# Kernel tuning notes

Measured on AMD Instinct MI355X. Metric: run time of the kernel, lower is better.

The kernel has to match this reference:

```python
import jax, jax.numpy as jnp
import numpy as np

BATCH = 1
SEQ = 3072
HID = 1024
HEADS = 16
HDIM = HID // HEADS  # 64
NSEQ = 8
SLEN = 380
ROPE_BASE = 10.0


def _boundaries():
    b, start = [], 0
    for _ in range(NSEQ):
        b.append((start, start + SLEN))
        start = start + SLEN + 1  # +1 for SEP token
    return b


def setup_inputs() -> dict:
    key = jax.random.key(0)
    ks = jax.random.split(key, 10)
    bnd = _boundaries()
    L = bnd[-1][1]  # actual_length = 3047
    # block-diagonal mask; SEP tokens attend only to themselves
    mask = np.zeros((L, L), dtype=bool)
    for s, e in bnd:
        mask[s:e, s:e] = True
    for s, e in bnd[:-1]:
        mask[e, e] = True
    # position ids reset at each sequence start
    pos = np.zeros((SEQ,), dtype=np.int32)
    for s, e in bnd:
        pos[s:e] = np.arange(e - s, dtype=np.int32)
    sc = 1.0 / np.sqrt(HID)
    return {
        "x": jax.random.normal(ks[0], (BATCH, SEQ, HID), jnp.float32),
        "wq": jax.random.normal(ks[1], (HID, HID), jnp.float32) * sc,
        "bq": jnp.zeros((HID,), jnp.float32),
        "wk": jax.random.normal(ks[2], (HID, HID), jnp.float32) * sc,
        "bk": jnp.zeros((HID,), jnp.float32),
        "wv": jax.random.normal(ks[3], (HID, HID), jnp.float32) * sc,
        "bv": jnp.zeros((HID,), jnp.float32),
        "wo": jax.random.normal(ks[4], (HID, HID), jnp.float32) * sc,
        "bo": jnp.zeros((HID,), jnp.float32),
        "mask": jnp.asarray(mask),
        "position_ids": jnp.asarray(pos)[None, :],  # [1, SEQ]
    }


def _apply_rope(q, k, pos):
    # q, k: [B, S, H, D]; pos: [B, S]
    half = HDIM // 2
    inv_freq = 1.0 / (ROPE_BASE ** (jnp.arange(0, HDIM, 2, dtype=jnp.float32) / HDIM))
    ang = pos.astype(jnp.float32)[..., None] * inv_freq  # [B, S, half]
    cos = jnp.cos(ang)[:, :, None, :]  # [B, S, 1, half]
    sin = jnp.sin(ang)[:, :, None, :]

    def rot(t):
        t1, t2 = t[..., :half], t[..., half:]
        return jnp.concatenate([t1 * cos - t2 * sin, t1 * sin + t2 * cos], axis=-1)

    return rot(q), rot(k)


def reference(x, wq, bq, wk, bk, wv, bv, wo, bo, mask, position_ids):
    B, S, _ = x.shape
    L = mask.shape[0]  # actual_length (static)
    q = (x @ wq.T + bq).reshape(B, S, HEADS, HDIM)
    k = (x @ wk.T + bk).reshape(B, S, HEADS, HDIM)
    v = (x @ wv.T + bv).reshape(B, S, HEADS, HDIM)
    q, k = _apply_rope(q, k, position_ids)
    # [B, H, S, D], trim to packed length
    q = q.transpose(0, 2, 1, 3)[:, :, :L, :]
    k = k.transpose(0, 2, 1, 3)[:, :, :L, :]
    v = v.transpose(0, 2, 1, 3)[:, :, :L, :]
    scores = jnp.einsum("bhqd,bhkd->bhqk", q, k) / jnp.sqrt(jnp.float32(HDIM))
    scores = jnp.where(mask[None, None], scores, -jnp.inf)
    attn = jax.nn.softmax(scores, axis=-1)
    out = jnp.einsum("bhqk,bhkd->bhqd", attn, v)  # [B, H, L, D]
    out = jnp.pad(out, ((0, 0), (0, 0), (0, S - L), (0, 0)))  # zero padded tail
    out = out.transpose(0, 2, 1, 3).reshape(B, S, HID)
    return out @ wo.T + bo
```

## Files before the change

kernel.cpp:

```cpp
#include <hip/hip_runtime.h>

typedef unsigned short u16;
typedef __attribute__((ext_vector_type(8))) short short8;
typedef __attribute__((ext_vector_type(4))) float f32x4;

#define SEQ 3072
#define HID 1024
#define HEADS 16
#define HDIM 64
#define SEGLEN 380
#define SEGSTR 381
#define NSEG 8
#define LTOT 3047
#define VPAD 384

static __device__ __forceinline__ u16 f2bf(float f) {
  unsigned u = __builtin_bit_cast(unsigned, f);
  u += 0x7fffu + ((u >> 16) & 1u);
  return (u16)(u >> 16);
}
static __device__ __forceinline__ float bf2f(u16 h) {
  unsigned u = ((unsigned)h) << 16;
  return __builtin_bit_cast(float, u);
}

static __device__ __forceinline__ void load_lds16(const void* g, void* l) {
  __builtin_amdgcn_global_load_lds((const __attribute__((address_space(1))) void*)g,
                                   (__attribute__((address_space(3))) void*)l, 16, 0, 0);
}

#define BAR() __builtin_amdgcn_s_barrier()
#define VM(N) asm volatile("s_waitcnt vmcnt(" #N ")" ::: "memory")

__global__ void cvt_all_kernel(const float* __restrict__ x, const float* __restrict__ wq,
                               const float* __restrict__ wk, const float* __restrict__ wv,
                               const float* __restrict__ wo, u16* __restrict__ out) {
  const int i = blockIdx.x * 256 + threadIdx.x;
  const float* s;
  int base;
  if (i < 786432)       { s = x;  base = 0; }
  else if (i < 1048576) { s = wq; base = 786432; }
  else if (i < 1310720) { s = wk; base = 1048576; }
  else if (i < 1572864) { s = wv; base = 1310720; }
  else                  { s = wo; base = 1572864; }
  float4 v = reinterpret_cast<const float4*>(s)[i - base];
  unsigned long long o = (unsigned long long)f2bf(v.x) |
                         ((unsigned long long)f2bf(v.y) << 16) |
                         ((unsigned long long)f2bf(v.z) << 32) |
                         ((unsigned long long)f2bf(v.w) << 48);
  reinterpret_cast<unsigned long long*>(out)[i] = o;
}

static __device__ __forceinline__ void stage_qkv(
    const u16* __restrict__ A, const u16* __restrict__ Bw,
    u16* As, u16* Bs, int rowBase, int colBase, int k0) {
  const int tid = threadIdx.x;
  const int w = tid >> 6;
#pragma unroll
  for (int c = 0; c < 2; ++c) {
    const int li = c * 512 + tid;
    const int row = li >> 3;
    const int j = (li & 7) ^ (row & 7);
    load_lds16(A + (size_t)(rowBase + row) * HID + k0 + j * 8, As + (c * 512 + w * 64) * 8);
    load_lds16(Bw + (size_t)(colBase + row) * HID + k0 + j * 8, Bs + (c * 512 + w * 64) * 8);
  }
}

static __device__ __forceinline__ void compute_qkv(
    const u16* As, const u16* Bs, int wr, int cb0, int lc, int lh, f32x4 (*acc)[2]) {
  short8 af[4][2], bfv[2][2];
#pragma unroll
  for (int m = 0; m < 4; ++m) {
    const int row = wr + m * 16 + lc;
#pragma unroll
    for (int ks = 0; ks < 2; ++ks)
      af[m][ks] = *reinterpret_cast<const short8*>(
          As + row * 64 + (((ks * 4 + lh) ^ (row & 7))) * 8);
  }
#pragma unroll
  for (int n = 0; n < 2; ++n) {
    const int row = cb0 + n * 32 + lc;
#pragma unroll
    for (int ks = 0; ks < 2; ++ks)
      bfv[n][ks] = *reinterpret_cast<const short8*>(
          Bs + row * 64 + (((ks * 4 + lh) ^ (row & 7))) * 8);
  }
  __builtin_amdgcn_s_setprio(1);
#pragma unroll
  for (int ks = 0; ks < 2; ++ks)
#pragma unroll
    for (int m = 0; m < 4; ++m)
#pragma unroll
      for (int n = 0; n < 2; ++n)
        acc[m][n] = __builtin_amdgcn_mfma_f32_16x16x32_bf16(af[m][ks], bfv[n][ks], acc[m][n], 0, 0, 0);
  __builtin_amdgcn_s_setprio(0);
}

__global__ __launch_bounds__(512) void qkv_gemm_kernel(
    const u16* __restrict__ xb,
    const u16* __restrict__ wqb, const u16* __restrict__ wkb, const u16* __restrict__ wvb,
    const float* __restrict__ bq, const float* __restrict__ bk, const float* __restrict__ bv,
    u16* __restrict__ qb, u16* __restrict__ kbuf, u16* __restrict__ vT) {
  __shared__ u16 As[2][128 * 64];
  __shared__ u16 Bs[2][128 * 64];
  const int which = blockIdx.y >> 3;
  const u16* Bw = (which == 0) ? wqb : (which == 1) ? wkb : wvb;
  const float* bias = (which == 0) ? bq : (which == 1) ? bk : bv;
  const int rowBase = blockIdx.x * 128;
  const int colBase = (blockIdx.y & 7) * 128;
  const int tid = threadIdx.x;
  const int w = tid >> 6, l = tid & 63, lc = l & 15, lh = l >> 4;
  const int wr = (w >> 2) * 64;
  const int c2 = w & 3;
  const int cb0 = (c2 >> 1) * 64 + (c2 & 1) * 16;

  f32x4 acc[4][2];
  f32x4 z4 = {0.f, 0.f, 0.f, 0.f};
#pragma unroll
  for (int m = 0; m < 4; ++m) { acc[m][0] = z4; acc[m][1] = z4; }

  stage_qkv(xb, Bw, As[0], Bs[0], rowBase, colBase, 0);
#pragma unroll 1
  for (int t = 0; t < 14; t += 2) {
    stage_qkv(xb, Bw, As[1], Bs[1], rowBase, colBase, (t + 1) * 64);
    VM(4); BAR();
    compute_qkv(As[0], Bs[0], wr, cb0, lc, lh, acc);
    BAR();
    stage_qkv(xb, Bw, As[0], Bs[0], rowBase, colBase, (t + 2) * 64);
    VM(4); BAR();
    compute_qkv(As[1], Bs[1], wr, cb0, lc, lh, acc);
    BAR();
  }
  stage_qkv(xb, Bw, As[1], Bs[1], rowBase, colBase, 15 * 64);
  VM(4); BAR();
  compute_qkv(As[0], Bs[0], wr, cb0, lc, lh, acc);
  BAR();
  VM(0); BAR();
  compute_qkv(As[1], Bs[1], wr, cb0, lc, lh, acc);

  const int f = (c2 & 1) * 16 + lc;
  const int col0 = colBase + (c2 >> 1) * 64 + f;
  if (which < 2) {
    u16* outp = which ? kbuf : qb;
    const float bv0 = bias[col0];
    const float bv1 = bias[col0 + 32];
    const float invf = exp2f(-(float)f * 0.10381025296523007f);
#pragma unroll
    for (int m = 0; m < 4; ++m) {
      const int row0 = rowBase + wr + m * 16 + lh * 4;
#pragma unroll
      for (int r = 0; r < 4; ++r) {
        const int row = row0 + r;
        const int rr = row % SEGSTR;
        const float pos = (float)((rr < SEGLEN) ? rr : 0);
        float sn, cs;
        sincosf(pos * invf, &sn, &cs);
        const float t1 = acc[m][0][r] + bv0;
        const float t2 = acc[m][1][r] + bv1;
        const size_t base = (size_t)row * HID + col0;
        outp[base] = f2bf(t1 * cs - t2 * sn);
        outp[base + 32] = f2bf(t1 * sn + t2 * cs);
      }
    }
  } else {
#pragma unroll
    for (int n = 0; n < 2; ++n) {
      const int col = col0 + n * 32;
      const float bvl = bias[col];
#pragma unroll
      for (int m = 0; m < 4; ++m) {
        const int row0 = rowBase + wr + m * 16 + lh * 4;
#pragma unroll
        for (int r = 0; r < 4; ++r) {
          const float v = acc[m][n][r] + bvl;
          const int row = row0 + r;
          const int sg = row / SEGSTR;
          const int j = row - sg * SEGSTR;
          if (sg < NSEG)
            vT[(size_t)col * (NSEG * VPAD) + sg * VPAD + j] = f2bf(v);
        }
      }
    }
  }
}

static __device__ __forceinline__ void stage_out(
    const u16* __restrict__ A, const u16* __restrict__ Bw,
    u16* As, u16* Bs, int rowBase, int colBase, int k0) {
  const int tid = threadIdx.x;
  const int w = tid >> 6;
#pragma unroll
  for (int c = 0; c < 2; ++c) {
    const int li = c * 512 + tid;
    const int row = li >> 3;
    const int j = (li & 7) ^ (row & 7);
    load_lds16(A + (size_t)(rowBase + row) * HID + k0 + j * 8,
               As + (c * 512 + w * 64) * 8);
  }
  {
    const int row = tid >> 3;
    const int j = (tid & 7) ^ (row & 7);
    load_lds16(Bw + (size_t)(colBase + row) * HID + k0 + j * 8, Bs + (w * 64) * 8);
  }
}

static __device__ __forceinline__ void compute_out(
    const u16* As, const u16* Bs, int wrO, int wcO, int lc, int lh, f32x4 (*acc)[2]) {
  short8 af[2][2], bfv[2][2];
#pragma unroll
  for (int m = 0; m < 2; ++m) {
    const int row = wrO + m * 16 + lc;
#pragma unroll
    for (int ks = 0; ks < 2; ++ks)
      af[m][ks] = *reinterpret_cast<const short8*>(
          As + row * 64 + (((ks * 4 + lh) ^ (row & 7))) * 8);
  }
#pragma unroll
  for (int n = 0; n < 2; ++n) {
    const int row = wcO + n * 16 + lc;
#pragma unroll
    for (int ks = 0; ks < 2; ++ks)
      bfv[n][ks] = *reinterpret_cast<const short8*>(
          Bs + row * 64 + (((ks * 4 + lh) ^ (row & 7))) * 8);
  }
  __builtin_amdgcn_s_setprio(1);
#pragma unroll
  for (int ks = 0; ks < 2; ++ks)
#pragma unroll
    for (int m = 0; m < 2; ++m)
#pragma unroll
      for (int n = 0; n < 2; ++n)
        acc[m][n] = __builtin_amdgcn_mfma_f32_16x16x32_bf16(af[m][ks], bfv[n][ks], acc[m][n], 0, 0, 0);
  __builtin_amdgcn_s_setprio(0);
}

__global__ __launch_bounds__(512) void out_gemm_kernel(
    const u16* __restrict__ aob, const u16* __restrict__ wob,
    const float* __restrict__ bo, float* __restrict__ out) {
  __shared__ u16 As[3][128 * 64];
  __shared__ u16 Bs[3][64 * 64];
  const int rowBase = blockIdx.x * 128;
  const int colBase = blockIdx.y * 64;
  const int tid = threadIdx.x;
  const int w = tid >> 6, l = tid & 63, lc = l & 15, lh = l >> 4;
  const int wrO = (w >> 1) * 32, wcO = (w & 1) * 32;
  f32x4 acc[2][2];
  f32x4 z4 = {0.f, 0.f, 0.f, 0.f};
#pragma unroll
  for (int m = 0; m < 2; ++m) { acc[m][0] = z4; acc[m][1] = z4; }

  stage_out(aob, wob, As[0], Bs[0], rowBase, colBase, 0);
  stage_out(aob, wob, As[1], Bs[1], rowBase, colBase, 64);
#pragma unroll 1
  for (int t = 0; t < 12; t += 3) {
    stage_out(aob, wob, As[2], Bs[2], rowBase, colBase, (t + 2) * 64);
    VM(6); BAR();
    compute_out(As[0], Bs[0], wrO, wcO, lc, lh, acc);
    BAR();
    stage_out(aob, wob, As[0], Bs[0], rowBase, colBase, (t + 3) * 64);
    VM(6); BAR();
    compute_out(As[1], Bs[1], wrO, wcO, lc, lh, acc);
    BAR();
    stage_out(aob, wob, As[1], Bs[1], rowBase, colBase, (t + 4) * 64);
    VM(6); BAR();
    compute_out(As[2], Bs[2], wrO, wcO, lc, lh, acc);
    BAR();
  }
  stage_out(aob, wob, As[2], Bs[2], rowBase, colBase, 14 * 64);
  VM(6); BAR();
  compute_out(As[0], Bs[0], wrO, wcO, lc, lh, acc);
  BAR();
  stage_out(aob, wob, As[0], Bs[0], rowBase, colBase, 15 * 64);
  VM(6); BAR();
  compute_out(As[1], Bs[1], wrO, wcO, lc, lh, acc);
  BAR();
  VM(3); BAR();
  compute_out(As[2], Bs[2], wrO, wcO, lc, lh, acc);
  BAR();
  VM(0); BAR();
  compute_out(As[0], Bs[0], wrO, wcO, lc, lh, acc);

#pragma unroll
  for (int n = 0; n < 2; ++n) {
    const int col = colBase + wcO + n * 16 + lc;
    const float bvl = bo[col];
#pragma unroll
    for (int m = 0; m < 2; ++m) {
      const int row0 = rowBase + wrO + m * 16 + lh * 4;
#pragma unroll
      for (int r = 0; r < 4; ++r)
        out[(size_t)(row0 + r) * HID + col] = acc[m][n][r] + bvl;
    }
  }
}

__global__ __launch_bounds__(256) void attn_kernel(
    const u16* __restrict__ qb, const u16* __restrict__ kb,
    const u16* __restrict__ vT, u16* __restrict__ ao) {
  __shared__ u16 Ks[3][32 * 64];
  __shared__ u16 Vs[3][64 * 32];
  __shared__ u16 P_lds[4][16 * 32];
  const int tid = threadIdx.x;
  const int w = tid >> 6, l = tid & 63, lc = l & 15, lh = l >> 4;
  const int W = (blockIdx.x & 7) * 96 + (blockIdx.x >> 3);
  const int qt = W % 6;
  const int seg = (W / 6) & 7;
  const int h = W / 48;
  const int segbase = seg * SEGSTR;
  const int rloc = qt * 64 + w * 16;

  const u16* qrow = qb + (size_t)(segbase + rloc + lc) * HID + h * HDIM + lh * 8;
  const short8 qf0 = *reinterpret_cast<const short8*>(qrow);
  const short8 qf1 = *reinterpret_cast<const short8*>(qrow + 32);

  const size_t vstride = (size_t)NSEG * VPAD;
  const u16* kseg = kb + (size_t)segbase * HID + h * HDIM;
  const u16* vseg = vT + (size_t)h * HDIM * vstride + seg * VPAD;

  const int krow = tid >> 3;
  const int kj = (tid & 7) ^ (krow & 7);
  const int vd = tid >> 2;
  const int vj = (tid & 3) ^ ((vd >> 2) & 3);

  f32x4 z4 = {0.f, 0.f, 0.f, 0.f};
  f32x4 accO[4] = {z4, z4, z4, z4};
  float psum[4] = {0.f, 0.f, 0.f, 0.f};

  u16* pl = &P_lds[w][0];
  int wo0[4], wo1[4];
#pragma unroll
  for (int r = 0; r < 4; ++r) {
    const int prow = lh * 4 + r;
    const int sw = (prow >> 1) & 3;
    wo0[r] = prow * 32 + ((lc >> 3) ^ sw) * 8 + (lc & 7);
    wo1[r] = prow * 32 + ((2 + (lc >> 3)) ^ sw) * 8 + (lc & 7);
  }
  const int prd_off = lc * 32 + (lh ^ ((lc >> 1) & 3)) * 8;

#define STAGE(B, T)                                                                 \
  load_lds16(kseg + (size_t)((T) * 32 + krow) * HID + kj * 8, &Ks[B][0] + w * 512); \
  load_lds16(vseg + (size_t)vd * vstride + (T) * 32 + vj * 8, &Vs[B][0] + w * 512);

#define STEP(B, MASKED)                                                               \
  {                                                                                   \
    const u16* KB = &Ks[B][0];                                                        \
    const u16* VB = &Vs[B][0];                                                        \
    const int ks0 = (lh ^ (lc & 7)) * 8;                                              \
    const int ks1 = ((lh + 4) ^ (lc & 7)) * 8;                                        \
    const short8 k00 = *reinterpret_cast<const short8*>(KB + lc * 64 + ks0);          \
    const short8 k01 = *reinterpret_cast<const short8*>(KB + lc * 64 + ks1);          \
    const short8 k10 = *reinterpret_cast<const short8*>(KB + (16 + lc) * 64 + ks0);   \
    const short8 k11 = *reinterpret_cast<const short8*>(KB + (16 + lc) * 64 + ks1);   \
    f32x4 s0 = z4, s1 = z4;                                                           \
    __builtin_amdgcn_s_setprio(1);                                                    \
    s0 = __builtin_amdgcn_mfma_f32_16x16x32_bf16(qf0, k00, s0, 0, 0, 0);              \
    s0 = __builtin_amdgcn_mfma_f32_16x16x32_bf16(qf1, k01, s0, 0, 0, 0);              \
    s1 = __builtin_amdgcn_mfma_f32_16x16x32_bf16(qf0, k10, s1, 0, 0, 0);              \
    s1 = __builtin_amdgcn_mfma_f32_16x16x32_bf16(qf1, k11, s1, 0, 0, 0);              \
    __builtin_amdgcn_s_setprio(0);                                                    \
    float p0[4], p1[4];                                                               \
    _Pragma("unroll") for (int r = 0; r < 4; ++r) {                                   \
      p0[r] = (!(MASKED) || lc < 28) ? __expf(s0[r] * 0.125f) : 0.f;                  \
      p1[r] = (!(MASKED) || lc < 12) ? __expf(s1[r] * 0.125f) : 0.f;                  \
      psum[r] += p0[r] + p1[r];                                                       \
    }                                                                                 \
    _Pragma("unroll") for (int r = 0; r < 4; ++r) {                                   \
      pl[wo0[r]] = f2bf(p0[r]);                                                       \
      pl[wo1[r]] = f2bf(p1[r]);                                                       \
    }                                                                                 \
    const short8 pf = *reinterpret_cast<const short8*>(pl + prd_off);                 \
    const int vsw = (lh ^ (lc >> 2)) * 8;                                             \
    const short8 v0 = *reinterpret_cast<const short8*>(VB + lc * 32 + vsw);           \
    const short8 v1 = *reinterpret_cast<const short8*>(VB + (16 + lc) * 32 + vsw);    \
    const short8 v2 = *reinterpret_cast<const short8*>(VB + (32 + lc) * 32 + vsw);    \
    const short8 v3 = *reinterpret_cast<const short8*>(VB + (48 + lc) * 32 + vsw);    \
    __builtin_amdgcn_s_setprio(1);                                                    \
    accO[0] = __builtin_amdgcn_mfma_f32_16x16x32_bf16(pf, v0, accO[0], 0, 0, 0);      \
    accO[1] = __builtin_amdgcn_mfma_f32_16x16x32_bf16(pf, v1, accO[1], 0, 0, 0);      \
    accO[2] = __builtin_amdgcn_mfma_f32_16x16x32_bf16(pf, v2, accO[2], 0, 0, 0);      \
    accO[3] = __builtin_amdgcn_mfma_f32_16x16x32_bf16(pf, v3, accO[3], 0, 0, 0);      \
    __builtin_amdgcn_s_setprio(0);                                                    \
  }

  STAGE(0, 0);
  STAGE(1, 1);
#pragma unroll 1
  for (int t = 0; t < 9; t += 3) {
    STAGE(2, t + 2);
    VM(4); BAR();
    STEP(0, false);
    BAR();
    STAGE(0, t + 3);
    VM(4); BAR();
    STEP(1, false);
    BAR();
    STAGE(1, t + 4);
    VM(4); BAR();
    STEP(2, false);
    BAR();
  }
  STAGE(2, 11);
  VM(4); BAR();
  STEP(0, false);
  BAR();
  VM(2); BAR();
  STEP(1, false);
  BAR();
  VM(0); BAR();
  STEP(2, true);
#undef STEP
#undef STAGE

  float inv[4];
#pragma unroll
  for (int r = 0; r < 4; ++r) {
    float s = psum[r];
    s += __shfl_xor(s, 1);
    s += __shfl_xor(s, 2);
    s += __shfl_xor(s, 4);
    s += __shfl_xor(s, 8);
    inv[r] = 1.0f / s;
  }
#pragma unroll
  for (int r = 0; r < 4; ++r) {
    const int lrow = rloc + lh * 4 + r;
    if (lrow < SEGLEN) {
      const size_t orow = (size_t)(segbase + lrow) * HID + h * HDIM;
#pragma unroll
      for (int n = 0; n < 4; ++n)
        ao[orow + n * 16 + lc] = f2bf(accO[n][r] * inv[r]);
    }
  }

  if (qt == 5) {
    if (seg < NSEG - 1) {
      if (tid < HDIM)
        ao[(size_t)(segbase + SEGLEN) * HID + h * HDIM + tid] =
            vT[(size_t)(h * HDIM + tid) * vstride + seg * VPAD + SEGLEN];
    } else {
#pragma unroll
      for (int k = 0; k < 7; ++k) {
        const int idx = k * 256 + tid;
        if (idx < 25 * HDIM) {
          const int rr = idx >> 6, cc = idx & 63;
          ao[(size_t)(LTOT + rr) * HID + h * HDIM + cc] = 0;
        }
      }
    }
  }
}

extern "C" void kernel_launch(void* const* d_in, const int* in_sizes, int n_in,
                              void* d_out, int out_size, void* d_ws, size_t ws_size,
                              hipStream_t stream) {
  const float* x  = (const float*)d_in[0];
  const float* wq = (const float*)d_in[1];
  const float* bq = (const float*)d_in[2];
  const float* wk = (const float*)d_in[3];
  const float* bk = (const float*)d_in[4];
  const float* wv = (const float*)d_in[5];
  const float* bv = (const float*)d_in[6];
  const float* wo = (const float*)d_in[7];
  const float* bo = (const float*)d_in[8];
  float* out = (float*)d_out;

  u16* ws = (u16*)d_ws;
  u16* xb   = ws;
  u16* wqb  = xb  + (size_t)SEQ * HID;
  u16* wkb  = wqb + (size_t)HID * HID;
  u16* wvb  = wkb + (size_t)HID * HID;
  u16* wob  = wvb + (size_t)HID * HID;
  u16* qb   = wob + (size_t)HID * HID;
  u16* kbuf = qb  + (size_t)SEQ * HID;
  u16* vT   = kbuf + (size_t)SEQ * HID;
  u16* aob  = vT  + (size_t)HID * (NSEG * VPAD);

  cvt_all_kernel<<<7168, 256, 0, stream>>>(x, wq, wk, wv, wo, ws);

  qkv_gemm_kernel<<<dim3(SEQ / 128, 24), 512, 0, stream>>>(
      xb, wqb, wkb, wvb, bq, bk, bv, qb, kbuf, vT);

  attn_kernel<<<768, 256, 0, stream>>>(qb, kbuf, vT, aob);

  out_gemm_kernel<<<dim3(SEQ / 128, HID / 64), 512, 0, stream>>>(aob, wob, bo, out);

  (void)in_sizes; (void)n_in; (void)out_size; (void)ws_size;
}
```

Measured before the change: 80.29 us.

## Enlarge QKV GEMM tile to 256x256 with phased staging over fused weights

The QKV projection GEMM moves from 128x128 tiles (576 blocks) to 256x256 tiles (144 blocks). The three weight matrices are treated as one contiguous 3072x1024 matrix, and each k-step's staging is split into four quarter loads interleaved with four MFMA phases. This raises arithmetic intensity and global-load reuse per block and hides load latency behind compute. The cost is 64 KB of LDS plus large accumulator register pressure (128 floats per thread), and only 144 blocks are launched, which may underfill the device's compute units.

```diff
diff --git a/kernel.cpp b/kernel.cpp
--- a/kernel.cpp
+++ b/kernel.cpp
@@ -51,9 +51,8 @@
   reinterpret_cast<unsigned long long*>(out)[i] = o;
 }
 
-static __device__ __forceinline__ void stage_qkv(
-    const u16* __restrict__ A, const u16* __restrict__ Bw,
-    u16* As, u16* Bs, int rowBase, int colBase, int k0) {
+static __device__ __forceinline__ void stage_half(
+    const u16* __restrict__ src, u16* dst, int base, int k0) {
   const int tid = threadIdx.x;
   const int w = tid >> 6;
 #pragma unroll
@@ -61,29 +60,30 @@
     const int li = c * 512 + tid;
     const int row = li >> 3;
     const int j = (li & 7) ^ (row & 7);
-    load_lds16(A + (size_t)(rowBase + row) * HID + k0 + j * 8, As + (c * 512 + w * 64) * 8);
-    load_lds16(Bw + (size_t)(colBase + row) * HID + k0 + j * 8, Bs + (c * 512 + w * 64) * 8);
-  }
-}
-
-static __device__ __forceinline__ void compute_qkv(
-    const u16* As, const u16* Bs, int wr, int cb0, int lc, int lh, f32x4 (*acc)[2]) {
-  short8 af[4][2], bfv[2][2];
+    load_lds16(src + (size_t)(base + row) * HID + k0 + j * 8,
+               dst + (c * 512 + w * 64) * 8);
+  }
+}
+
+static __device__ __forceinline__ void phase_mfma(
+    const u16* At, const u16* Bt, int wrow, int wcol, int lc, int lh,
+    int mq, int nq, f32x4 (*acc)[4]) {
+  short8 af[4][2], bf[2][2];
 #pragma unroll
   for (int m = 0; m < 4; ++m) {
-    const int row = wr + m * 16 + lc;
+    const int row = wrow + mq * 64 + m * 16 + lc;
 #pragma unroll
     for (int ks = 0; ks < 2; ++ks)
       af[m][ks] = *reinterpret_cast<const short8*>(
-          As + row * 64 + (((ks * 4 + lh) ^ (row & 7))) * 8);
+          At + row * 64 + (((ks * 4 + lh) ^ (row & 7)) * 8));
   }
 #pragma unroll
   for (int n = 0; n < 2; ++n) {
-    const int row = cb0 + n * 32 + lc;
+    const int row = wcol + nq * 32 + n * 16 + lc;
 #pragma unroll
     for (int ks = 0; ks < 2; ++ks)
-      bfv[n][ks] = *reinterpret_cast<const short8*>(
-          Bs + row * 64 + (((ks * 4 + lh) ^ (row & 7))) * 8);
+      bf[n][ks] = *reinterpret_cast<const short8*>(
+          Bt + row * 64 + (((ks * 4 + lh) ^ (row & 7)) * 8));
   }
   __builtin_amdgcn_s_setprio(1);
 #pragma unroll
@@ -92,92 +92,120 @@
     for (int m = 0; m < 4; ++m)
 #pragma unroll
       for (int n = 0; n < 2; ++n)
-        acc[m][n] = __builtin_amdgcn_mfma_f32_16x16x32_bf16(af[m][ks], bfv[n][ks], acc[m][n], 0, 0, 0);
+        acc[mq * 4 + m][nq * 2 + n] = __builtin_amdgcn_mfma_f32_16x16x32_bf16(
+            af[m][ks], bf[n][ks], acc[mq * 4 + m][nq * 2 + n], 0, 0, 0);
   __builtin_amdgcn_s_setprio(0);
 }
 
-__global__ __launch_bounds__(512) void qkv_gemm_kernel(
-    const u16* __restrict__ xb,
-    const u16* __restrict__ wqb, const u16* __restrict__ wkb, const u16* __restrict__ wvb,
+__global__ __launch_bounds__(512, 2) void qkv_gemm_kernel(
+    const u16* __restrict__ xb, const u16* __restrict__ wall,
     const float* __restrict__ bq, const float* __restrict__ bk, const float* __restrict__ bv,
     u16* __restrict__ qb, u16* __restrict__ kbuf, u16* __restrict__ vT) {
-  __shared__ u16 As[2][128 * 64];
-  __shared__ u16 Bs[2][128 * 64];
-  const int which = blockIdx.y >> 3;
-  const u16* Bw = (which == 0) ? wqb : (which == 1) ? wkb : wvb;
-  const float* bias = (which == 0) ? bq : (which == 1) ? bk : bv;
-  const int rowBase = blockIdx.x * 128;
-  const int colBase = (blockIdx.y & 7) * 128;
+  __shared__ u16 Abuf[2][256 * 64];
+  __shared__ u16 Bbuf[2][256 * 64];
+  const int bx = blockIdx.x, by = blockIdx.y;
+  const int rowBase = bx * 256;
+  const int gcb = by * 256;
   const int tid = threadIdx.x;
   const int w = tid >> 6, l = tid & 63, lc = l & 15, lh = l >> 4;
-  const int wr = (w >> 2) * 64;
-  const int c2 = w & 3;
-  const int cb0 = (c2 >> 1) * 64 + (c2 & 1) * 16;
-
-  f32x4 acc[4][2];
+  const int wm = w >> 2, wn = w & 3;
+  const int wrow = wm * 128, wcol = wn * 64;
+
+  f32x4 acc[8][4];
   f32x4 z4 = {0.f, 0.f, 0.f, 0.f};
 #pragma unroll
-  for (int m = 0; m < 4; ++m) { acc[m][0] = z4; acc[m][1] = z4; }
-
-  stage_qkv(xb, Bw, As[0], Bs[0], rowBase, colBase, 0);
+  for (int m = 0; m < 8; ++m)
+#pragma unroll
+    for (int n = 0; n < 4; ++n) acc[m][n] = z4;
+
+  stage_half(xb, Abuf[0], rowBase, 0);
+  stage_half(xb, Abuf[0] + 8192, rowBase + 128, 0);
+  stage_half(wall, Bbuf[0], gcb, 0);
+  stage_half(wall, Bbuf[0] + 8192, gcb + 128, 0);
+
 #pragma unroll 1
-  for (int t = 0; t < 14; t += 2) {
-    stage_qkv(xb, Bw, As[1], Bs[1], rowBase, colBase, (t + 1) * 64);
-    VM(4); BAR();
-    compute_qkv(As[0], Bs[0], wr, cb0, lc, lh, acc);
-    BAR();
-    stage_qkv(xb, Bw, As[0], Bs[0], rowBase, colBase, (t + 2) * 64);
-    VM(4); BAR();
-    compute_qkv(As[1], Bs[1], wr, cb0, lc, lh, acc);
-    BAR();
-  }
-  stage_qkv(xb, Bw, As[1], Bs[1], rowBase, colBase, 15 * 64);
-  VM(4); BAR();
-  compute_qkv(As[0], Bs[0], wr, cb0, lc, lh, acc);
-  BAR();
-  VM(0); BAR();
-  compute_qkv(As[1], Bs[1], wr, cb0, lc, lh, acc);
-
-  const int f = (c2 & 1) * 16 + lc;
-  const int col0 = colBase + (c2 >> 1) * 64 + f;
+  for (int t = 0; t < 15; ++t) {
+    const int cur = t & 1;
+    const int k1 = (t + 1) * 64;
+    const u16* At = Abuf[cur];
+    const u16* Bt = Bbuf[cur];
+    u16* An = Abuf[cur ^ 1];
+    u16* Bn = Bbuf[cur ^ 1];
+    stage_half(xb, An, rowBase, k1);
+    VM(2); BAR();
+    phase_mfma(At, Bt, wrow, wcol, lc, lh, 0, 0, acc);
+    BAR();
+    stage_half(xb, An + 8192, rowBase + 128, k1);
+    phase_mfma(At, Bt, wrow, wcol, lc, lh, 0, 1, acc);
+    BAR();
+    stage_half(wall, Bn, gcb, k1);
+    phase_mfma(At, Bt, wrow, wcol, lc, lh, 1, 0, acc);
+    BAR();
+    stage_half(wall, Bn + 8192, gcb + 128, k1);
+    phase_mfma(At, Bt, wrow, wcol, lc, lh, 1, 1, acc);
+    BAR();
+  }
+  {
+    const u16* At = Abuf[1];
+    const u16* Bt = Bbuf[1];
+    VM(0); BAR();
+    phase_mfma(At, Bt, wrow, wcol, lc, lh, 0, 0, acc);
+    BAR();
+    phase_mfma(At, Bt, wrow, wcol, lc, lh, 0, 1, acc);
+    BAR();
+    phase_mfma(At, Bt, wrow, wcol, lc, lh, 1, 0, acc);
+    BAR();
+    phase_mfma(At, Bt, wrow, wcol, lc, lh, 1, 1, acc);
+  }
+
+  const int which = by >> 2;
+  const int colWb = (by & 3) * 256 + wcol;
   if (which < 2) {
     u16* outp = which ? kbuf : qb;
-    const float bv0 = bias[col0];
-    const float bv1 = bias[col0 + 32];
-    const float invf = exp2f(-(float)f * 0.10381025296523007f);
-#pragma unroll
-    for (int m = 0; m < 4; ++m) {
-      const int row0 = rowBase + wr + m * 16 + lh * 4;
+    const float* bias = which ? bk : bq;
+    const float bv0 = bias[colWb + lc];
+    const float bv1 = bias[colWb + 16 + lc];
+    const float bv2 = bias[colWb + 32 + lc];
+    const float bv3 = bias[colWb + 48 + lc];
+    const float invf0 = exp2f(-(float)lc * 0.10381025296523007f);
+    const float invf1 = exp2f(-(float)(16 + lc) * 0.10381025296523007f);
+#pragma unroll
+    for (int m = 0; m < 8; ++m) {
+      const int row0 = rowBase + wrow + m * 16 + lh * 4;
 #pragma unroll
       for (int r = 0; r < 4; ++r) {
         const int row = row0 + r;
         const int rr = row % SEGSTR;
         const float pos = (float)((rr < SEGLEN) ? rr : 0);
-        float sn, cs;
-        sincosf(pos * invf, &sn, &cs);
-        const float t1 = acc[m][0][r] + bv0;
-        const float t2 = acc[m][1][r] + bv1;
-        const size_t base = (size_t)row * HID + col0;
-        outp[base] = f2bf(t1 * cs - t2 * sn);
-        outp[base + 32] = f2bf(t1 * sn + t2 * cs);
+        float sn0, cs0, sn1, cs1;
+        sincosf(pos * invf0, &sn0, &cs0);
+        sincosf(pos * invf1, &sn1, &cs1);
+        const float a0 = acc[m][0][r] + bv0;
+        const float a1 = acc[m][1][r] + bv1;
+        const float a2 = acc[m][2][r] + bv2;
+        const float a3 = acc[m][3][r] + bv3;
+        const size_t base = (size_t)row * HID + colWb;
+        outp[base + lc]      = f2bf(a0 * cs0 - a2 * sn0);
+        outp[base + 32 + lc] = f2bf(a0 * sn0 + a2 * cs0);
+        outp[base + 16 + lc] = f2bf(a1 * cs1 - a3 * sn1);
+        outp[base + 48 + lc] = f2bf(a1 * sn1 + a3 * cs1);
       }
     }
   } else {
 #pragma unroll
-    for (int n = 0; n < 2; ++n) {
-      const int col = col0 + n * 32;
-      const float bvl = bias[col];
-#pragma unroll
-      for (int m = 0; m < 4; ++m) {
-        const int row0 = rowBase + wr + m * 16 + lh * 4;
+    for (int n = 0; n < 4; ++n) {
+      const int col = colWb + n * 16 + lc;
+      const float bvl = bv[col];
+#pragma unroll
+      for (int m = 0; m < 8; ++m) {
+        const int row0 = rowBase + wrow + m * 16 + lh * 4;
 #pragma unroll
         for (int r = 0; r < 4; ++r) {
-          const float v = acc[m][n][r] + bvl;
           const int row = row0 + r;
           const int sg = row / SEGSTR;
           const int j = row - sg * SEGSTR;
           if (sg < NSEG)
-            vT[(size_t)col * (NSEG * VPAD) + sg * VPAD + j] = f2bf(v);
+            vT[(size_t)col * (NSEG * VPAD) + sg * VPAD + j] = f2bf(acc[m][n][r] + bvl);
         }
       }
     }
@@ -467,9 +495,7 @@
   u16* ws = (u16*)d_ws;
   u16* xb   = ws;
   u16* wqb  = xb  + (size_t)SEQ * HID;
-  u16* wkb  = wqb + (size_t)HID * HID;
-  u16* wvb  = wkb + (size_t)HID * HID;
-  u16* wob  = wvb + (size_t)HID * HID;
+  u16* wob  = wqb + (size_t)3 * HID * HID;
   u16* qb   = wob + (size_t)HID * HID;
   u16* kbuf = qb  + (size_t)SEQ * HID;
   u16* vT   = kbuf + (size_t)SEQ * HID;
@@ -477,8 +503,8 @@
 
   cvt_all_kernel<<<7168, 256, 0, stream>>>(x, wq, wk, wv, wo, ws);
 
-  qkv_gemm_kernel<<<dim3(SEQ / 128, 24), 512, 0, stream>>>(
-      xb, wqb, wkb, wvb, bq, bk, bv, qb, kbuf, vT);
+  qkv_gemm_kernel<<<dim3(12, 12), 512, 0, stream>>>(
+      xb, wqb, bq, bk, bv, qb, kbuf, vT);
 
   attn_kernel<<<768, 256, 0, stream>>>(qb, kbuf, vT, aob);
 
```

Result: slower. 130.1 us (+62.0%).
